# Optimization experiments

Measured on AMD Instinct MI355X. Metric: run time of the kernel, lower is better.

Reference implementation:

```python
import jax, jax.numpy as jnp
import numpy as np

D = 1024
L_COMP = 16384
L_FULL = 32768
EPS = 1e-4


def setup_inputs() -> dict:
    key = jax.random.key(0)
    k1, k2 = jax.random.split(key)
    x = jax.random.normal(k1, (1, L_COMP, D), dtype=jnp.float32)
    p_selected = jax.random.uniform(k2, (L_COMP,), dtype=jnp.float32)
    # boundary mask over full sequence: exactly L_COMP ones, first position forced to 1
    rng = np.random.default_rng(0)
    pos = np.concatenate([[0], np.sort(rng.choice(np.arange(1, L_FULL), L_COMP - 1, replace=False))])
    b_np = np.zeros((1, L_FULL), dtype=np.int32)
    b_np[0, pos] = 1
    b = jnp.asarray(b_np)
    return {"x": x, "p_selected": p_selected, "b": b}


def _ema_scan(x, p):
    # z_t = (1 - p_t) * z_{t-1} + p_t * x_t  (exact math of the mamba chunk scan
    # with A=-1, dt=log(1/(1-p)), B=p, C=1, x pre-divided by dt)
    a = jnp.broadcast_to((1.0 - p)[None, :, None], x.shape)  # (1, L, d) decay
    bxt = p[None, :, None] * x                                # (1, L, d) input term

    def combine(c1, c2):
        a1, b1 = c1
        a2, b2 = c2
        return a1 * a2, a2 * b1 + b2

    _, z = jax.lax.associative_scan(combine, (a, bxt), axis=1)
    return z


def reference(x, p_selected, b):
    p = jnp.clip(p_selected.astype(jnp.float32), EPS, 1.0 - EPS)  # (L_comp,)
    z_bar = _ema_scan(x.astype(jnp.float32), p)                   # (1, L_comp, d)
    plug_back_idx = jnp.cumsum(b, axis=1) - 1                     # (1, L_full)
    out = jnp.take(z_bar[0], plug_back_idx[0], axis=0)[None]      # (1, L_full, d)
    return out.astype(x.dtype)
```

## Files before the change

### kernel.cpp

```cpp
#include <hip/hip_runtime.h>


#define DCH 1024
#define L_COMP 16384
#define L_FULL 32768
#define CHUNK 32
#define NCHUNK (L_COMP / CHUNK)
#define SEG (L_FULL / NCHUNK)
#define EPSV 1e-4f

typedef float v4f __attribute__((ext_vector_type(4)));

__device__ __forceinline__ float clipp(float p) {
    p = fmaxf(p, EPSV);
    return fminf(p, 1.0f - EPSV);
}

__global__ __launch_bounds__(256, 2) void chunk_kernel(
    const float* __restrict__ x, const float* __restrict__ p,
    const int* __restrict__ b,
    float* __restrict__ Bbuf, float* __restrict__ Abuf, int* __restrict__ bsum) {
    const int c = blockIdx.x;
    const int tid = threadIdx.x;
    const int lane = tid & 63;
    const int wave = tid >> 6;
    const int base = c * CHUNK;

    const v4f* x4 = reinterpret_cast<const v4f*>(x) + (size_t)base * (DCH / 4) + tid;
    v4f h = (v4f)0.f;
    float aprod = 1.0f;
    for (int ib = 0; ib < CHUNK; ib += 8) {
        v4f xv[8];
        float pv[8];
#pragma unroll
        for (int j = 0; j < 8; ++j) {
            xv[j] = x4[(ib + j) * (DCH / 4)];
            pv[j] = clipp(p[base + ib + j]);
        }
#pragma unroll
        for (int j = 0; j < 8; ++j) {
            float a = 1.0f - pv[j];
            h = a * h + pv[j] * xv[j];
            aprod *= a;
        }
    }
    reinterpret_cast<v4f*>(Bbuf)[c * (DCH / 4) + tid] = h;
    if (tid == 0) Abuf[c] = aprod;
    if (wave == 0) {
        int v = b[c * SEG + lane];
        int s = v;
#pragma unroll
        for (int off = 1; off < 64; off <<= 1) s += __shfl_xor(s, off, 64);
        if (lane == 0) bsum[c] = s;
    }
}

#define BATCHB 32
__global__ __launch_bounds__(64) void interchunk_kernel(
    const float* __restrict__ Bbuf, const float* __restrict__ Abuf,
    float* __restrict__ Hbuf) {
    const int ch4 = blockIdx.x * 64 + threadIdx.x;
    const v4f* B4 = reinterpret_cast<const v4f*>(Bbuf) + ch4;
    v4f* H4 = reinterpret_cast<v4f*>(Hbuf) + ch4;
    v4f h = (v4f)0.f;
    for (int cb = 0; cb < NCHUNK; cb += BATCHB) {
        v4f bv[BATCHB];
        float av[BATCHB];
#pragma unroll
        for (int j = 0; j < BATCHB; ++j) {
            bv[j] = B4[(cb + j) * (DCH / 4)];
            av[j] = Abuf[cb + j];
        }
#pragma unroll
        for (int j = 0; j < BATCHB; ++j) {
            H4[(cb + j) * (DCH / 4)] = h;
            h = av[j] * h + bv[j];
        }
    }
}

__global__ __launch_bounds__(256, 2) void dechunk_kernel(
    const float* __restrict__ x, const float* __restrict__ p,
    const int* __restrict__ b, float* __restrict__ out,
    const float* __restrict__ Hbuf, const int* __restrict__ bsum) {
    const int c = blockIdx.x;
    const int tid = threadIdx.x;
    const int lane = tid & 63;
    const int wave = tid >> 6;
    const int base = c * CHUNK;

    __shared__ int bpref[NCHUNK + 1];
    __shared__ int spos[CHUNK + 1];
    __shared__ int wtot[4];

    {
        int v0 = bsum[2 * tid];
        int v1 = bsum[2 * tid + 1];
        int s = v0 + v1;
        int incl = s;
#pragma unroll
        for (int off = 1; off < 64; off <<= 1) {
            int n = __shfl_up(incl, off, 64);
            if (lane >= off) incl += n;
        }
        if (lane == 63) wtot[wave] = incl;
        __syncthreads();
        int woff = 0;
        for (int w = 0; w < wave; ++w) woff += wtot[w];
        int ex = woff + incl - s;
        bpref[2 * tid] = ex;
        bpref[2 * tid + 1] = ex + v0;
        if (tid == 0) bpref[NCHUNK] = L_COMP;
        __syncthreads();
    }

    if (tid <= CHUNK) {
        int t = base + tid;
        int posv = L_FULL;
        if (t < L_COMP) {
            int lo = 0, hi = NCHUNK;
            while (hi - lo > 1) {
                int mid = (lo + hi) >> 1;
                if (bpref[mid] <= t) lo = mid; else hi = mid;
            }
            int lr = t - bpref[lo];
            const int4* bseg = reinterpret_cast<const int4*>(b) + lo * (SEG / 4);
            int cnt = 0;
#pragma unroll 4
            for (int q = 0; q < SEG / 4; ++q) {
                int4 w = bseg[q];
                if (w.x) { if (cnt == lr) posv = lo * SEG + 4 * q + 0; ++cnt; }
                if (w.y) { if (cnt == lr) posv = lo * SEG + 4 * q + 1; ++cnt; }
                if (w.z) { if (cnt == lr) posv = lo * SEG + 4 * q + 2; ++cnt; }
                if (w.w) { if (cnt == lr) posv = lo * SEG + 4 * q + 3; ++cnt; }
            }
        }
        spos[tid] = posv;
    }
    __syncthreads();

    {
        const v4f* x4 = reinterpret_cast<const v4f*>(x) + (size_t)base * (DCH / 4) + tid;
        v4f* out4 = reinterpret_cast<v4f*>(out) + tid;
        v4f h = reinterpret_cast<const v4f*>(Hbuf)[c * (DCH / 4) + tid];
        int f0 = spos[0];
        for (int ib = 0; ib < CHUNK; ib += 8) {
            v4f xv[8];
            float pv[8];
            int fe[8];
#pragma unroll
            for (int j = 0; j < 8; ++j) {
                xv[j] = x4[(ib + j) * (DCH / 4)];
                pv[j] = clipp(p[base + ib + j]);
                fe[j] = spos[ib + j + 1];
            }
#pragma unroll
            for (int j = 0; j < 8; ++j) {
                float a = 1.0f - pv[j];
                h = a * h + pv[j] * xv[j];
                for (int f = f0; f < fe[j]; ++f) {
                    out4[(size_t)f * (DCH / 4)] = h;
                }
                f0 = fe[j];
            }
        }
    }
}

extern "C" void kernel_launch(void* const* d_in, const int* in_sizes, int n_in,
                              void* d_out, int out_size, void* d_ws, size_t ws_size,
                              hipStream_t stream) {
    const float* x = (const float*)d_in[0];
    const float* p = (const float*)d_in[1];
    const int* b = (const int*)d_in[2];
    float* out = (float*)d_out;

    char* ws = (char*)d_ws;
    float* Abuf = (float*)ws;
    int* bsum = (int*)(ws + 4096);
    float* Bbuf = (float*)(ws + 8192);
    float* Hbuf = Bbuf + (size_t)NCHUNK * DCH;

    chunk_kernel<<<NCHUNK, 256, 0, stream>>>(x, p, b, Bbuf, Abuf, bsum);
    interchunk_kernel<<<4, 64, 0, stream>>>(Bbuf, Abuf, Hbuf);
    dechunk_kernel<<<NCHUNK, 256, 0, stream>>>(x, p, b, out, Hbuf, bsum);
}
```

Measured before the change: 234.9 us.

## Fuse inter-chunk scan into dechunk kernel by recomputing prefix per block

Removes the separate serial inter-chunk scan kernel, which ran on only four small blocks. Each dechunk block now folds all preceding chunk summaries itself to obtain its starting state. This trades a kernel launch and a latency-bound serial pass for redundant quadratic reads of the chunk summary buffer, which are expected to hit in L2. Output stores also become nontemporal to avoid polluting cache.

```diff
diff --git a/kernel.cpp b/kernel.cpp
--- a/kernel.cpp
+++ b/kernel.cpp
@@ -55,34 +55,11 @@
     }
 }
 
-#define BATCHB 32
-__global__ __launch_bounds__(64) void interchunk_kernel(
-    const float* __restrict__ Bbuf, const float* __restrict__ Abuf,
-    float* __restrict__ Hbuf) {
-    const int ch4 = blockIdx.x * 64 + threadIdx.x;
-    const v4f* B4 = reinterpret_cast<const v4f*>(Bbuf) + ch4;
-    v4f* H4 = reinterpret_cast<v4f*>(Hbuf) + ch4;
-    v4f h = (v4f)0.f;
-    for (int cb = 0; cb < NCHUNK; cb += BATCHB) {
-        v4f bv[BATCHB];
-        float av[BATCHB];
-#pragma unroll
-        for (int j = 0; j < BATCHB; ++j) {
-            bv[j] = B4[(cb + j) * (DCH / 4)];
-            av[j] = Abuf[cb + j];
-        }
-#pragma unroll
-        for (int j = 0; j < BATCHB; ++j) {
-            H4[(cb + j) * (DCH / 4)] = h;
-            h = av[j] * h + bv[j];
-        }
-    }
-}
-
 __global__ __launch_bounds__(256, 2) void dechunk_kernel(
     const float* __restrict__ x, const float* __restrict__ p,
     const int* __restrict__ b, float* __restrict__ out,
-    const float* __restrict__ Hbuf, const int* __restrict__ bsum) {
+    const float* __restrict__ Bbuf, const float* __restrict__ Abuf,
+    const int* __restrict__ bsum) {
     const int c = blockIdx.x;
     const int tid = threadIdx.x;
     const int lane = tid & 63;
@@ -137,12 +114,33 @@
         }
         spos[tid] = posv;
     }
+
+    v4f h = (v4f)0.f;
+    {
+        const v4f* B4 = reinterpret_cast<const v4f*>(Bbuf) + tid;
+        int k = 0;
+        for (; k + 16 <= c; k += 16) {
+            v4f bv[16];
+            float av[16];
+#pragma unroll
+            for (int j = 0; j < 16; ++j) {
+                bv[j] = B4[(k + j) * (DCH / 4)];
+                av[j] = Abuf[k + j];
+            }
+#pragma unroll
+            for (int j = 0; j < 16; ++j)
+                h = av[j] * h + bv[j];
+        }
+        for (; k < c; ++k) {
+            v4f bv = B4[k * (DCH / 4)];
+            h = Abuf[k] * h + bv;
+        }
+    }
     __syncthreads();
 
     {
         const v4f* x4 = reinterpret_cast<const v4f*>(x) + (size_t)base * (DCH / 4) + tid;
         v4f* out4 = reinterpret_cast<v4f*>(out) + tid;
-        v4f h = reinterpret_cast<const v4f*>(Hbuf)[c * (DCH / 4) + tid];
         int f0 = spos[0];
         for (int ib = 0; ib < CHUNK; ib += 8) {
             v4f xv[8];
@@ -159,7 +157,7 @@
                 float a = 1.0f - pv[j];
                 h = a * h + pv[j] * xv[j];
                 for (int f = f0; f < fe[j]; ++f) {
-                    out4[(size_t)f * (DCH / 4)] = h;
+                    __builtin_nontemporal_store(h, &out4[(size_t)f * (DCH / 4)]);
                 }
                 f0 = fe[j];
             }
@@ -179,9 +177,7 @@
     float* Abuf = (float*)ws;
     int* bsum = (int*)(ws + 4096);
     float* Bbuf = (float*)(ws + 8192);
-    float* Hbuf = Bbuf + (size_t)NCHUNK * DCH;
 
     chunk_kernel<<<NCHUNK, 256, 0, stream>>>(x, p, b, Bbuf, Abuf, bsum);
-    interchunk_kernel<<<4, 64, 0, stream>>>(Bbuf, Abuf, Hbuf);
-    dechunk_kernel<<<NCHUNK, 256, 0, stream>>>(x, p, b, out, Hbuf, bsum);
+    dechunk_kernel<<<NCHUNK, 256, 0, stream>>>(x, p, b, out, Bbuf, Abuf, bsum);
 }
```

New measurement: 212.1 us. 9.7% less time.
